# Performance work log

Hardware: AMD Instinct MI355X
Metric: run time of the kernel (lower is better)

## Reference

```python
import jax, jax.numpy as jnp
import numpy as np

B, T, N_INP, N_HID = 128, 2048, 512, 512

def _xavier(key, fan_in, fan_out):
    limit = jnp.sqrt(6.0 / (fan_in + fan_out)).astype(jnp.float32)
    return jax.random.uniform(key, (fan_in, fan_out), jnp.float32, -limit, limit)

def setup_inputs() -> dict:
    key = jax.random.key(0)
    k1, k2, k3 = jax.random.split(key, 3)
    return {
        "inputs": jax.random.normal(k1, (B, T, N_INP), jnp.float32),
        "H0": jnp.zeros((B, N_HID), jnp.float32),
        "W_xh": _xavier(k2, N_INP, N_HID),
        "W_hh": _xavier(k3, N_HID, N_HID),
        "b_h": jnp.zeros((N_HID,), jnp.float32),
    }

def reference(inputs, H0, W_xh, W_hh, b_h):
    # Precompute input projection for all timesteps (same math as per-step matmul):
    # x_proj: [T, B, n_hid]
    x_proj = jnp.einsum('bti,ih->tbh', inputs, W_xh) + b_h

    def step(H_t, xp_t):
        H_t = jnp.tanh(xp_t + H_t @ W_hh)  # [B, n_hid]
        return H_t, H_t

    H_T, outs = jax.lax.scan(step, H0, x_proj)  # outs: [T, B, n_hid]
    return jnp.swapaxes(outs, 0, 1), H_T
```

## Files before the change

kernel.cpp:

```cpp
#include <hip/hip_runtime.h>
#include <hip/hip_bf16.h>
#include <hip/hip_fp16.h>
#include <math.h>

#define B_SZ 128
#define T_SZ 2048
#define NI 512
#define NH 512

typedef _Float16 h2_t __attribute__((ext_vector_type(2)));

__device__ __forceinline__ float dot2p(unsigned w, unsigned h, float acc) {
#if __has_builtin(__builtin_amdgcn_fdot2)
    return __builtin_amdgcn_fdot2(__builtin_bit_cast(h2_t, w),
                                  __builtin_bit_cast(h2_t, h), acc, false);
#else
    const h2_t wv = __builtin_bit_cast(h2_t, w);
    const h2_t hv = __builtin_bit_cast(h2_t, h);
    acc = fmaf((float)wv.x, (float)hv.x, acc);
    acc = fmaf((float)wv.y, (float)hv.y, acc);
    return acc;
#endif
}

#define DOT_BLK(WV, HV)                      \
    do {                                     \
        acc = dot2p((WV).x, (HV).x, acc);    \
        acc = dot2p((WV).y, (HV).y, acc);    \
        acc = dot2p((WV).z, (HV).z, acc);    \
        acc = dot2p((WV).w, (HV).w, acc);    \
    } while (0)

__global__ __launch_bounds__(256) void pack_whh(
    const float* __restrict__ W, uint4* __restrict__ wt3)
{
    const int idx = blockIdx.x * 256 + threadIdx.x;
    const int j   = idx & 511;
    const int kk4 = idx >> 9;
    const int k0  = kk4 * 8;
    unsigned d[4];
    #pragma unroll
    for (int q = 0; q < 4; ++q) {
        const unsigned lo =
            __half_as_ushort(__float2half_rn(W[(size_t)(k0 + 2 * q)     * NH + j]));
        const unsigned hi =
            __half_as_ushort(__float2half_rn(W[(size_t)(k0 + 2 * q + 1) * NH + j]));
        d[q] = lo | (hi << 16);
    }
    wt3[idx] = make_uint4(d[0], d[1], d[2], d[3]);
}

#define BM 64
#define BN 64
#define BK 16

__global__ __launch_bounds__(256) void proj_gemm(
    const float* __restrict__ A,
    const float* __restrict__ W,
    const float* __restrict__ bias,
    float* __restrict__ C)
{
    __shared__ float As[BK][BM];
    __shared__ float Bs[BK][BN];
    const int m0 = blockIdx.y * BM;
    const int n0 = blockIdx.x * BN;
    const int tid = threadIdx.x;
    const int tx = tid & 15;
    const int ty = tid >> 4;

    const int ar = tid >> 2;
    const int ac = (tid & 3) * 4;
    const int bk = tid >> 4;
    const int bn = (tid & 15) * 4;

    float acc[4][4] = {};

    for (int k0 = 0; k0 < NI; k0 += BK) {
        float4 av = *reinterpret_cast<const float4*>(
            &A[(size_t)(m0 + ar) * NI + k0 + ac]);
        float4 bv = *reinterpret_cast<const float4*>(
            &W[(size_t)(k0 + bk) * NH + n0 + bn]);
        __syncthreads();
        As[ac + 0][ar] = av.x;
        As[ac + 1][ar] = av.y;
        As[ac + 2][ar] = av.z;
        As[ac + 3][ar] = av.w;
        *reinterpret_cast<float4*>(&Bs[bk][bn]) = bv;
        __syncthreads();
        #pragma unroll
        for (int kk = 0; kk < BK; ++kk) {
            float a[4], b[4];
            #pragma unroll
            for (int i = 0; i < 4; ++i) a[i] = As[kk][ty * 4 + i];
            #pragma unroll
            for (int jj = 0; jj < 4; ++jj) b[jj] = Bs[kk][tx * 4 + jj];
            #pragma unroll
            for (int i = 0; i < 4; ++i)
                #pragma unroll
                for (int jj = 0; jj < 4; ++jj)
                    acc[i][jj] = fmaf(a[i], b[jj], acc[i][jj]);
        }
    }

    #pragma unroll
    for (int i = 0; i < 4; ++i) {
        const size_t row = (size_t)(m0 + ty * 4 + i);
        #pragma unroll
        for (int jj = 0; jj < 4; ++jj) {
            const int col = n0 + tx * 4 + jj;
            C[row * NH + col] = acc[i][jj] + bias[col];
        }
    }
}

__global__ __launch_bounds__(1024, 4) void rnn_scan_d(
    const uint4* wt3,
    const float* __restrict__ H0,
    float* out,
    float* hT)
{
    __shared__ uint4   wlds[16][512];
    __shared__ unsigned hpk[2][256];
    __shared__ float    ps[NH];

    const int tid  = threadIdx.x;
    const int b    = blockIdx.x;
    const int j    = tid & 511;
    const int half = tid >> 9;

    #pragma unroll
    for (int pass = 0; pass < 8; ++pass) {
        const int idx = pass * 1024 + tid;
        const int r   = idx >> 9;
        const int col = idx & 511;
        const int gb  = (r >> 3) * 32 + (r & 7);
        wlds[r][col] = wt3[(size_t)gb * 512 + col];
    }

    if (tid < NH) {
        const float h0v = H0[(size_t)b * NH + tid];
        const float h0o = __shfl_down(h0v, 1);
        if ((tid & 1) == 0) {
            const unsigned lo = __half_as_ushort(__float2half_rn(h0v));
            const unsigned hi = __half_as_ushort(__float2half_rn(h0o));
            hpk[0][tid >> 1] = lo | (hi << 16);
        }
    }
    __syncthreads();

    float* outrow = out + (size_t)b * T_SZ * NH + tid;
    float xp_cur = (tid < NH) ? outrow[0] : 0.f;
    int cur = 0;
    float hv = 0.f;

    const uint4* wstr = wt3 + (size_t)(half * 32 + 8) * 512 + j;
    const int wr0 = half * 8;

    for (int t = 0; t < T_SZ; ++t) {
        float xp_next = 0.f;
        if (tid < NH && t + 1 < T_SZ)
            xp_next = __builtin_nontemporal_load(outrow + (size_t)(t + 1) * NH);

        const uint4* hq = reinterpret_cast<const uint4*>(hpk[cur]) + half * 32;
        float acc = 0.f;

        #pragma unroll
        for (int g = 0; g < 8; ++g) {
            {
                const uint4 wv = wlds[wr0 + g][j];
                const uint4 hb = hq[g];
                DOT_BLK(wv, hb);
            }
            #pragma unroll
            for (int s = 0; s < 3; ++s) {
                const int sb = g * 3 + s;
                const uint4 wv = wstr[(size_t)sb * 512];
                const uint4 hb = hq[8 + sb];
                DOT_BLK(wv, hb);
            }
        }

        if (half == 1) ps[j] = acc;
        __syncthreads();

        if (tid < NH) {
            hv = tanhf(acc + ps[tid] + xp_cur);
            __builtin_nontemporal_store(hv, outrow + (size_t)t * NH);
            const float ho = __shfl_down(hv, 1);
            if ((tid & 1) == 0) {
                const unsigned lo = __half_as_ushort(__float2half_rn(hv));
                const unsigned hi = __half_as_ushort(__float2half_rn(ho));
                hpk[cur ^ 1][tid >> 1] = lo | (hi << 16);
            }
            xp_cur = xp_next;
        }
        __syncthreads();
        cur ^= 1;
    }
    if (tid < NH) hT[(size_t)b * NH + tid] = hv;
}

extern "C" void kernel_launch(void* const* d_in, const int* in_sizes, int n_in,
                              void* d_out, int out_size, void* d_ws, size_t ws_size,
                              hipStream_t stream) {
    const float* inputs = (const float*)d_in[0];
    const float* H0     = (const float*)d_in[1];
    const float* W_xh   = (const float*)d_in[2];
    const float* W_hh   = (const float*)d_in[3];
    const float* b_h    = (const float*)d_in[4];

    float* out = (float*)d_out;
    float* hT  = out + (size_t)B_SZ * T_SZ * NH;

    uint4* wt3 = (uint4*)d_ws;

    pack_whh<<<128, 256, 0, stream>>>(W_hh, wt3);

    dim3 g1(NH / BN, (B_SZ * T_SZ) / BM);
    proj_gemm<<<g1, 256, 0, stream>>>(inputs, W_xh, b_h, out);

    rnn_scan_d<<<128, 1024, 0, stream>>>(wt3, H0, out, hT);
}
```

Baseline: 9.528 ms.

## Replace FP32 SIMT input-projection GEMM with fp16 MFMA GEMM

```diff
diff --git a/kernel.cpp b/kernel.cpp
--- a/kernel.cpp
+++ b/kernel.cpp
@@ -7,8 +7,11 @@
 #define T_SZ 2048
 #define NI 512
 #define NH 512
-
-typedef _Float16 h2_t __attribute__((ext_vector_type(2)));
+#define M_TOT (B_SZ * T_SZ)
+
+typedef _Float16 h2_t  __attribute__((ext_vector_type(2)));
+typedef _Float16 f16x8 __attribute__((ext_vector_type(8)));
+typedef float    f32x4 __attribute__((ext_vector_type(4)));
 
 __device__ __forceinline__ float dot2p(unsigned w, unsigned h, float acc) {
 #if __has_builtin(__builtin_amdgcn_fdot2)
@@ -31,6 +34,11 @@
         acc = dot2p((WV).w, (HV).w, acc);    \
     } while (0)
 
+__device__ __forceinline__ unsigned pkh2(float a, float b) {
+    return (unsigned)__half_as_ushort(__float2half_rn(a)) |
+           ((unsigned)__half_as_ushort(__float2half_rn(b)) << 16);
+}
+
 __global__ __launch_bounds__(256) void pack_whh(
     const float* __restrict__ W, uint4* __restrict__ wt3)
 {
@@ -40,77 +48,124 @@
     const int k0  = kk4 * 8;
     unsigned d[4];
     #pragma unroll
-    for (int q = 0; q < 4; ++q) {
-        const unsigned lo =
-            __half_as_ushort(__float2half_rn(W[(size_t)(k0 + 2 * q)     * NH + j]));
-        const unsigned hi =
-            __half_as_ushort(__float2half_rn(W[(size_t)(k0 + 2 * q + 1) * NH + j]));
-        d[q] = lo | (hi << 16);
-    }
+    for (int q = 0; q < 4; ++q)
+        d[q] = pkh2(W[(size_t)(k0 + 2 * q) * NH + j],
+                    W[(size_t)(k0 + 2 * q + 1) * NH + j]);
     wt3[idx] = make_uint4(d[0], d[1], d[2], d[3]);
 }
 
-#define BM 64
-#define BN 64
-#define BK 16
-
-__global__ __launch_bounds__(256) void proj_gemm(
-    const float* __restrict__ A,
-    const float* __restrict__ W,
+__global__ __launch_bounds__(256) void transpose_w(
+    const float* __restrict__ W, char* __restrict__ wT)
+{
+    __shared__ float tile[64][65];
+    const int kt = blockIdx.x & 7, nt = blockIdx.x >> 3;
+    const int t  = threadIdx.x;
+    #pragma unroll
+    for (int r = 0; r < 4; ++r) {
+        const int kl = r * 16 + (t >> 4);
+        const int nl = (t & 15) * 4;
+        const float4 v = *reinterpret_cast<const float4*>(
+            &W[(size_t)(kt * 64 + kl) * NH + nt * 64 + nl]);
+        tile[kl][nl + 0] = v.x; tile[kl][nl + 1] = v.y;
+        tile[kl][nl + 2] = v.z; tile[kl][nl + 3] = v.w;
+    }
+    __syncthreads();
+    #pragma unroll
+    for (int r = 0; r < 4; ++r) {
+        const int nl  = r * 16 + (t >> 4);
+        const int kl4 = (t & 15) * 4;
+        uint2 u;
+        u.x = pkh2(tile[kl4 + 0][nl], tile[kl4 + 1][nl]);
+        u.y = pkh2(tile[kl4 + 2][nl], tile[kl4 + 3][nl]);
+        *reinterpret_cast<uint2*>(
+            wT + (size_t)(nt * 64 + nl) * 1024 + (size_t)(kt * 64 + kl4) * 2) = u;
+    }
+}
+
+__global__ __launch_bounds__(256) void proj_mfma(
+    const float* __restrict__ inp,
+    const char* __restrict__ wT,
     const float* __restrict__ bias,
     float* __restrict__ C)
 {
-    __shared__ float As[BK][BM];
-    __shared__ float Bs[BK][BN];
-    const int m0 = blockIdx.y * BM;
-    const int n0 = blockIdx.x * BN;
-    const int tid = threadIdx.x;
-    const int tx = tid & 15;
-    const int ty = tid >> 4;
-
-    const int ar = tid >> 2;
-    const int ac = (tid & 3) * 4;
-    const int bk = tid >> 4;
-    const int bn = (tid & 15) * 4;
-
-    float acc[4][4] = {};
-
-    for (int k0 = 0; k0 < NI; k0 += BK) {
-        float4 av = *reinterpret_cast<const float4*>(
-            &A[(size_t)(m0 + ar) * NI + k0 + ac]);
-        float4 bv = *reinterpret_cast<const float4*>(
-            &W[(size_t)(k0 + bk) * NH + n0 + bn]);
-        __syncthreads();
-        As[ac + 0][ar] = av.x;
-        As[ac + 1][ar] = av.y;
-        As[ac + 2][ar] = av.z;
-        As[ac + 3][ar] = av.w;
-        *reinterpret_cast<float4*>(&Bs[bk][bn]) = bv;
+    __shared__ ushort As[64][72];
+    __shared__ ushort Bs[256][72];
+    const int tid  = threadIdx.x;
+    const int w    = tid >> 6;
+    const int lane = tid & 63;
+    const int l15  = lane & 15, l16 = lane >> 4;
+    const int m0   = blockIdx.y * 64;
+    const int n0   = blockIdx.x * 256;
+
+    f32x4 acc[4][4] = {};
+
+    float bc[4];
+    #pragma unroll
+    for (int fc = 0; fc < 4; ++fc)
+        bc[fc] = bias[n0 + w * 64 + fc * 16 + l15];
+
+    for (int ks = 0; ks < 8; ++ks) {
+        __syncthreads();
+        {
+            const int r = tid >> 2, q = tid & 3;
+            const float* src = inp + (size_t)(m0 + r) * NI + ks * 64 + q * 16;
+            const float4 v0 = *reinterpret_cast<const float4*>(src + 0);
+            const float4 v1 = *reinterpret_cast<const float4*>(src + 4);
+            const float4 v2 = *reinterpret_cast<const float4*>(src + 8);
+            const float4 v3 = *reinterpret_cast<const float4*>(src + 12);
+            uint4 ua, ub;
+            ua.x = pkh2(v0.x, v0.y); ua.y = pkh2(v0.z, v0.w);
+            ua.z = pkh2(v1.x, v1.y); ua.w = pkh2(v1.z, v1.w);
+            ub.x = pkh2(v2.x, v2.y); ub.y = pkh2(v2.z, v2.w);
+            ub.z = pkh2(v3.x, v3.y); ub.w = pkh2(v3.z, v3.w);
+            *reinterpret_cast<uint4*>(&As[r][q * 16 + 0]) = ua;
+            *reinterpret_cast<uint4*>(&As[r][q * 16 + 8]) = ub;
+        }
+        {
+            const uint4* src = reinterpret_cast<const uint4*>(
+                wT + (size_t)(n0 + tid) * 1024 + ks * 128);
+            const uint4 b0 = src[0], b1 = src[1], b2 = src[2], b3 = src[3];
+            const uint4 b4 = src[4], b5 = src[5], b6 = src[6], b7 = src[7];
+            *reinterpret_cast<uint4*>(&Bs[tid][ 0]) = b0;
+            *reinterpret_cast<uint4*>(&Bs[tid][ 8]) = b1;
+            *reinterpret_cast<uint4*>(&Bs[tid][16]) = b2;
+            *reinterpret_cast<uint4*>(&Bs[tid][24]) = b3;
+            *reinterpret_cast<uint4*>(&Bs[tid][32]) = b4;
+            *reinterpret_cast<uint4*>(&Bs[tid][40]) = b5;
+            *reinterpret_cast<uint4*>(&Bs[tid][48]) = b6;
+            *reinterpret_cast<uint4*>(&Bs[tid][56]) = b7;
+        }
         __syncthreads();
         #pragma unroll
-        for (int kk = 0; kk < BK; ++kk) {
-            float a[4], b[4];
-            #pragma unroll
-            for (int i = 0; i < 4; ++i) a[i] = As[kk][ty * 4 + i];
-            #pragma unroll
-            for (int jj = 0; jj < 4; ++jj) b[jj] = Bs[kk][tx * 4 + jj];
-            #pragma unroll
-            for (int i = 0; i < 4; ++i)
+        for (int kh = 0; kh < 2; ++kh) {
+            f16x8 a[4], b[4];
+            #pragma unroll
+            for (int fr = 0; fr < 4; ++fr)
+                a[fr] = *reinterpret_cast<const f16x8*>(
+                    &As[fr * 16 + l15][kh * 32 + l16 * 8]);
+            #pragma unroll
+            for (int fc = 0; fc < 4; ++fc)
+                b[fc] = *reinterpret_cast<const f16x8*>(
+                    &Bs[w * 64 + fc * 16 + l15][kh * 32 + l16 * 8]);
+            #pragma unroll
+            for (int fr = 0; fr < 4; ++fr)
                 #pragma unroll
-                for (int jj = 0; jj < 4; ++jj)
-                    acc[i][jj] = fmaf(a[i], b[jj], acc[i][jj]);
-        }
-    }
-
-    #pragma unroll
-    for (int i = 0; i < 4; ++i) {
-        const size_t row = (size_t)(m0 + ty * 4 + i);
+                for (int fc = 0; fc < 4; ++fc)
+                    acc[fr][fc] = __builtin_amdgcn_mfma_f32_16x16x32_f16(
+                        a[fr], b[fc], acc[fr][fc], 0, 0, 0);
+        }
+    }
+
+    #pragma unroll
+    for (int fr = 0; fr < 4; ++fr)
         #pragma unroll
-        for (int jj = 0; jj < 4; ++jj) {
-            const int col = n0 + tx * 4 + jj;
-            C[row * NH + col] = acc[i][jj] + bias[col];
-        }
-    }
+        for (int fc = 0; fc < 4; ++fc)
+            #pragma unroll
+            for (int i = 0; i < 4; ++i) {
+                const int row = m0 + fr * 16 + l16 * 4 + i;
+                const int col = n0 + w * 64 + fc * 16 + l15;
+                C[(size_t)row * NH + col] = acc[fr][fc][i] + bc[fc];
+            }
 }
 
 __global__ __launch_bounds__(1024, 4) void rnn_scan_d(
@@ -140,11 +195,8 @@
     if (tid < NH) {
         const float h0v = H0[(size_t)b * NH + tid];
         const float h0o = __shfl_down(h0v, 1);
-        if ((tid & 1) == 0) {
-            const unsigned lo = __half_as_ushort(__float2half_rn(h0v));
-            const unsigned hi = __half_as_ushort(__float2half_rn(h0o));
-            hpk[0][tid >> 1] = lo | (hi << 16);
-        }
+        if ((tid & 1) == 0)
+            hpk[0][tid >> 1] = pkh2(h0v, h0o);
     }
     __syncthreads();
 
@@ -187,11 +239,8 @@
             hv = tanhf(acc + ps[tid] + xp_cur);
             __builtin_nontemporal_store(hv, outrow + (size_t)t * NH);
             const float ho = __shfl_down(hv, 1);
-            if ((tid & 1) == 0) {
-                const unsigned lo = __half_as_ushort(__float2half_rn(hv));
-                const unsigned hi = __half_as_ushort(__float2half_rn(ho));
-                hpk[cur ^ 1][tid >> 1] = lo | (hi << 16);
-            }
+            if ((tid & 1) == 0)
+                hpk[cur ^ 1][tid >> 1] = pkh2(hv, ho);
             xp_cur = xp_next;
         }
         __syncthreads();
@@ -212,12 +261,15 @@
     float* out = (float*)d_out;
     float* hT  = out + (size_t)B_SZ * T_SZ * NH;
 
+    char*  wTb = (char*)d_ws;
     uint4* wt3 = (uint4*)d_ws;
 
+    transpose_w<<<64, 256, 0, stream>>>(W_xh, wTb);
+
+    proj_mfma<<<dim3(NH / 256, M_TOT / 64), 256, 0, stream>>>(
+        inputs, wTb, b_h, out);
+
     pack_whh<<<128, 256, 0, stream>>>(W_hh, wt3);
 
-    dim3 g1(NH / BN, (B_SZ * T_SZ) / BM);
-    proj_gemm<<<g1, 256, 0, stream>>>(inputs, W_xh, b_h, out);
-
     rnn_scan_d<<<128, 1024, 0, stream>>>(wt3, H0, out, hT);
 }
```

After: 7.903 ms (median of 2 runs). 1.21x faster.
